# Performance work log

Hardware: AMD Instinct MI355X
Metric: run time of the kernel (lower is better)

## Reference

```python
import jax, jax.numpy as jnp
import numpy as np

N = 20000      # nodes
E = 400000     # edges
D = 256        # input_dim == hidden_dim
L = 4          # num_layers
EIN = 32       # edgenet_input_dim // 2
EH = 128       # edge parser hidden
NC = 2         # num_classes
JK = L * D     # 1024
BN_EPS = 1e-5


def setup_inputs() -> dict:
    key = jax.random.key(0)
    ks = jax.random.split(key, 16)
    s = 0.05
    inp = {
        "features": jax.random.normal(ks[0], (N, D), jnp.float32),
        "edge_index": jax.random.randint(ks[1], (2, E), 0, N, dtype=jnp.int64),
        "edgenet_input": jax.random.normal(ks[2], (E, 2 * EIN), jnp.float32),
        # ChebConv weights: [layer, k, in, out] (all layers 256->256, K=3, no bias)
        "cheb_w": jax.random.normal(ks[3], (L, 3, D, D), jnp.float32) * s,
        # EdgeEncoder (PAE-style) parser: Linear(32,128)+ReLU+BN+Linear(128,128)
        "en_w1": jax.random.normal(ks[4], (EIN, EH), jnp.float32) * s,
        "en_b1": jnp.zeros((EH,), jnp.float32),
        "en_g1": jnp.ones((EH,), jnp.float32),
        "en_be1": jnp.zeros((EH,), jnp.float32),
        "en_w2": jax.random.normal(ks[5], (EH, EH), jnp.float32) * s,
        "en_b2": jnp.zeros((EH,), jnp.float32),
        # cls head: Linear(1024,256)+ReLU+BN(256)+Linear(256,2)
        "cls_w1": jax.random.normal(ks[6], (JK, 256), jnp.float32) * s,
        "cls_b1": jnp.zeros((256,), jnp.float32),
        "cls_g": jnp.ones((256,), jnp.float32),
        "cls_b": jnp.zeros((256,), jnp.float32),
        "cls_w2": jax.random.normal(ks[7], (256, NC), jnp.float32) * s,
        "cls_b2": jnp.zeros((NC,), jnp.float32),
    }
    return inp


def _bn_eval(x, g, b):
    # eval-mode BatchNorm1d with fresh running stats (mean=0, var=1)
    return x * (g / jnp.sqrt(1.0 + BN_EPS)) + b


def reference(features, edge_index, edgenet_input, cheb_w,
              en_w1, en_b1, en_g1, en_be1, en_w2, en_b2,
              cls_w1, cls_b1, cls_g, cls_b, cls_w2, cls_b2):
    row, col = edge_index[0], edge_index[1]

    # ---- EdgeEncoder (PAE): shared parser on both halves + cosine sim ----
    def parser(x):
        h = jnp.maximum(x @ en_w1 + en_b1, 0.0)
        h = _bn_eval(h, en_g1, en_be1)
        return h @ en_w2 + en_b2

    half = edgenet_input.shape[1] // 2
    h1 = parser(edgenet_input[:, :half])
    h2 = parser(edgenet_input[:, half:])
    n1 = jnp.maximum(jnp.linalg.norm(h1, axis=1), 1e-8)
    n2 = jnp.maximum(jnp.linalg.norm(h2, axis=1), 1e-8)
    cos = jnp.sum(h1 * h2, axis=1) / (n1 * n2)
    edge_weight = (cos + 1.0) * 0.5  # [E]

    # ---- ChebConv sym normalization (lambda_max=2): L_hat = -D^-1/2 A D^-1/2 ----
    deg = jax.ops.segment_sum(edge_weight, row, num_segments=N)
    dis = jnp.where(deg > 0, jax.lax.rsqrt(jnp.maximum(deg, 1e-30)), 0.0)
    norm = -dis[row] * edge_weight * dis[col]  # [E]

    def prop(x):  # out[col] += norm * x[row]
        return jax.ops.segment_sum(x[row] * norm[:, None], col, num_segments=N)

    # ---- stacked ChebConv (K=3, no bias) + ReLU + JK concat ----
    x = features
    jk = None
    for i in range(L):
        W = cheb_w[i]
        Tx0 = x
        Tx1 = prop(Tx0)
        Tx2 = 2.0 * prop(Tx1) - Tx0
        h = jnp.maximum(Tx0 @ W[0] + Tx1 @ W[1] + Tx2 @ W[2], 0.0)
        jk = h if i == 0 else jnp.concatenate([jk, h], axis=1)
        x = h

    # ---- cls head ----
    z = jnp.maximum(jk @ cls_w1 + cls_b1, 0.0)
    z = _bn_eval(z, cls_g, cls_b)
    logit = z @ cls_w2 + cls_b2
    return (logit, edge_weight)
```

## Files before the change

### kernel.cpp

```cpp
#include <hip/hip_runtime.h>
#include <hip/hip_bf16.h>

#define NN 20000
#define EE 400000
#define RSBN 0.9999950000374997f

typedef __attribute__((ext_vector_type(8))) short short8;
typedef __attribute__((ext_vector_type(8))) unsigned short ushort8;
typedef __attribute__((ext_vector_type(4))) short bf4;
typedef __attribute__((ext_vector_type(4))) float floatx4;

__device__ __forceinline__ short f2bf(float f) {
  union { float f; unsigned u; } v; v.f = f;
  unsigned r = v.u + 0x7fffu + ((v.u >> 16) & 1u);
  return (short)(r >> 16);
}
__device__ __forceinline__ unsigned f2bf2(float x, float y) {
  union { __hip_bfloat162 h; unsigned u; } v;
  v.h = __float22bfloat162_rn(make_float2(x, y));
  return v.u;
}
__device__ __forceinline__ float bf2f(unsigned short u) {
  union { unsigned u; float f; } v; v.u = ((unsigned)u) << 16;
  return v.f;
}
__device__ __forceinline__ void gl_lds16(const void* g, void* l) {
  __builtin_amdgcn_global_load_lds(
      (const __attribute__((address_space(1))) unsigned*)g,
      (__attribute__((address_space(3))) unsigned*)l, 16, 0, 0);
}

__device__ __forceinline__ floatx4 mfma16(bf4 a, bf4 b, floatx4 c) {
#if __has_builtin(__builtin_amdgcn_mfma_f32_16x16x16bf16_1k)
  return __builtin_amdgcn_mfma_f32_16x16x16bf16_1k(a, b, c, 0, 0, 0);
#else
  floatx4 d;
  asm volatile("v_mfma_f32_16x16x16_bf16 %0, %1, %2, %3"
               : "=&v"(d) : "v"(a), "v"(b), "v"(c));
  return d;
#endif
}

__global__ __launch_bounds__(256) void ewconv_kernel(
    const float* __restrict__ w1, const float* __restrict__ w2,
    const float* __restrict__ g1, const float* __restrict__ be1,
    const float* __restrict__ b1, const float* __restrict__ b2,
    unsigned short* __restrict__ ewf)
{
  int tid = threadIdx.x;
#pragma unroll
  for (int i = 0; i < 16; i++) {
    int idx = i * 256 + tid;
    int k = idx >> 7, n = idx & 127;
    int pos = ((n >> 4) * 64 + (k >> 3) * 16 + (n & 15)) * 8 + (k & 7);
    ewf[pos] = f2bf(w1[idx]);
  }
#pragma unroll
  for (int i = 0; i < 64; i++) {
    int idx = i * 256 + tid;
    int k = idx >> 7, n = idx & 127;
    int u = k >> 4, q = (k >> 2) & 3, j = k & 3;
    int t = n >> 4, l = n & 15;
    int pos = (((u * 8 + t) * 4 + q) * 16 + l) * 4 + j;
    ewf[4096 + pos] = f2bf(w2[idx] * g1[k] * RSBN);
  }
  float* fb = (float*)(ewf + 20480);
  if (tid < 128) {
    fb[tid] = b1[tid];
    float acc = b2[tid];
    for (int k = 0; k < 128; k++) acc += be1[k] * w2[k * 128 + tid] * g1[k] * RSBN;
    fb[128 + tid] = acc;
  }
}

__global__ __launch_bounds__(512, 6) void edge_kernel(
    const float* __restrict__ xin, const int* __restrict__ eidx,
    const unsigned short* __restrict__ ewf,
    float* __restrict__ ew_out,
    float* __restrict__ deg, int* __restrict__ cnt)
{
  __shared__ short wbuf[20992];

  int tid = threadIdx.x;
  int lane = tid & 63;
  int wv = tid >> 6;
  int l15 = lane & 15;
  int quad = lane >> 4;

#pragma unroll
  for (int i = 0; i < 5; i++)
    gl_lds16(ewf + (i * 512 + tid) * 8, &wbuf[(i * 512 + tid) * 8]);
  if (tid < 64)
    gl_lds16(ewf + (2560 + tid) * 8, &wbuf[(2560 + tid) * 8]);

  const short* w1f = wbuf;
  const short* w2f = wbuf + 4096;

  int rowbase = blockIdx.x * 128 + wv * 16;

  short8 af;
  {
    const float* xp = xin + (size_t)(rowbase + l15) * 32 + quad * 8;
    float4 v0 = *(const float4*)xp;
    float4 v1 = *(const float4*)(xp + 4);
    union { short8 s; unsigned u[4]; } a;
    a.u[0] = f2bf2(v0.x, v0.y); a.u[1] = f2bf2(v0.z, v0.w);
    a.u[2] = f2bf2(v1.x, v1.y); a.u[3] = f2bf2(v1.z, v1.w);
    af = a.s;
  }

  __syncthreads();

  const float* fb = (const float*)(wbuf + 20480);

  floatx4 acc1[8];
#pragma unroll
  for (int t = 0; t < 8; t++) {
    floatx4 z = *(const floatx4*)&fb[t * 16 + quad * 4];
    acc1[t] = __builtin_amdgcn_mfma_f32_16x16x32_bf16(
        *(const short8*)&w1f[(t * 64 + lane) * 8], af, z, 0, 0, 0);
  }

  bf4 pb[8];
#pragma unroll
  for (int u = 0; u < 8; u++) {
    union { bf4 s; unsigned w[2]; } o;
    o.w[0] = f2bf2(fmaxf(acc1[u][0], 0.f), fmaxf(acc1[u][1], 0.f));
    o.w[1] = f2bf2(fmaxf(acc1[u][2], 0.f), fmaxf(acc1[u][3], 0.f));
    pb[u] = o.s;
  }

  floatx4 acc2[8];
#pragma unroll
  for (int t = 0; t < 8; t++)
    acc2[t] = *(const floatx4*)&fb[128 + t * 16 + quad * 4];
#pragma unroll
  for (int u = 0; u < 8; u++)
#pragma unroll
    for (int t = 0; t < 8; t++) {
      bf4 a4 = *(const bf4*)&w2f[((u * 8 + t) * 64 + lane) * 4];
      acc2[t] = mfma16(a4, pb[u], acc2[t]);
    }

  float qq = 0.f, pp = 0.f;
#pragma unroll
  for (int t = 0; t < 8; t++)
#pragma unroll
    for (int r = 0; r < 4; r++) {
      float h = acc2[t][r];
      float hp = __shfl_xor(h, 1, 64);
      qq += h * h;
      pp += h * hp;
    }
  qq += __shfl_xor(qq, 16, 64);
  pp += __shfl_xor(pp, 16, 64);
  qq += __shfl_xor(qq, 32, 64);
  pp += __shfl_xor(pp, 32, 64);
  float rr = __shfl_xor(qq, 1, 64);

  if (quad == 0 && !(l15 & 1)) {
    int e = (rowbase + l15) >> 1;
    float n1 = fmaxf(sqrtf(qq), 1e-8f);
    float n2 = fmaxf(sqrtf(rr), 1e-8f);
    float w = (pp / (n1 * n2) + 1.f) * 0.5f;
    ew_out[e] = w;
    atomicAdd(deg + eidx[e], w);
    atomicAdd(cnt + eidx[EE + e], 1);
  }
}

__global__ __launch_bounds__(256) void fconv_kernel(const float* __restrict__ src,
                                                    unsigned short* __restrict__ dst) {
  size_t i = ((size_t)blockIdx.x * 256 + threadIdx.x) * 8;
  float4 a = *(const float4*)(src + i);
  float4 b = *(const float4*)(src + i + 4);
  union { ushort8 s; unsigned u[4]; } o;
  o.u[0] = f2bf2(a.x, a.y); o.u[1] = f2bf2(a.z, a.w);
  o.u[2] = f2bf2(b.x, b.y); o.u[3] = f2bf2(b.z, b.w);
  *(ushort8*)(dst + i) = o.s;
}

__global__ __launch_bounds__(256) void wconv_kernel(
    const float* __restrict__ cheb_w, const float* __restrict__ cls_w1,
    unsigned short* __restrict__ wtc, unsigned short* __restrict__ clsT)
{
  __shared__ unsigned short tile[64][80];
  int z = blockIdx.z;
  const float* src; unsigned short* dst; int ldk;
  if (z < 12) {
    int l = z / 3, c = z % 3;
    src = cheb_w + (size_t)z * 65536;
    dst = wtc + (size_t)l * 196608 + c * 256;
    ldk = 768;
  } else {
    int c = z - 12;
    src = cls_w1 + (size_t)c * 65536;
    dst = clsT + c * 256;
    ldk = 1024;
  }
  int t = threadIdx.x;
  int k0 = blockIdx.x * 64, n0 = blockIdx.y * 64;
#pragma unroll
  for (int pass = 0; pass < 4; pass++) {
    int kk = pass * 16 + (t >> 4);
    int nl = (t & 15) * 4;
    float4 v = *(const float4*)(src + (size_t)(k0 + kk) * 256 + n0 + nl);
    tile[nl + 0][kk] = f2bf(v.x);
    tile[nl + 1][kk] = f2bf(v.y);
    tile[nl + 2][kk] = f2bf(v.z);
    tile[nl + 3][kk] = f2bf(v.w);
  }
  __syncthreads();
  int nl = t >> 2, kc = (t & 3) * 16;
  ushort8 v0 = *(const ushort8*)&tile[nl][kc];
  ushort8 v1 = *(const ushort8*)&tile[nl][kc + 8];
  unsigned short* dp = dst + (size_t)(n0 + nl) * ldk + k0 + kc;
  *(ushort8*)dp = v0;
  *(ushort8*)(dp + 8) = v1;
}

__global__ __launch_bounds__(1024) void scan_kernel(const int* __restrict__ cnt, int* __restrict__ ptr) {
  __shared__ int sums[1024];
  int tid = threadIdx.x;
  const int n = NN;
  const int chunk = (n + 1023) / 1024;
  int base = tid * chunk;
  int s = 0;
  for (int i = 0; i < chunk; i++) {
    int idx = base + i;
    if (idx < n) s += (cnt[idx] + 3) & ~3;
  }
  sums[tid] = s;
  __syncthreads();
  for (int off = 1; off < 1024; off <<= 1) {
    int v = (tid >= off) ? sums[tid - off] : 0;
    __syncthreads();
    sums[tid] += v;
    __syncthreads();
  }
  int run = (tid == 0) ? 0 : sums[tid - 1];
  for (int i = 0; i < chunk; i++) {
    int idx = base + i;
    if (idx < n) { ptr[idx] = run; run += (cnt[idx] + 3) & ~3; }
  }
  if (tid == 1023) ptr[n] = run;
}

__global__ void fill_kernel(const int* __restrict__ eidx, const float* __restrict__ ew,
                            const float* __restrict__ deg, const int* __restrict__ ptr,
                            int* __restrict__ fill, int* __restrict__ cidx, float* __restrict__ cval) {
  int e = blockIdx.x * 256 + threadIdx.x;
  if (e < EE) {
    int r = eidx[e], c = eidx[EE + e];
    float dr = deg[r], dc = deg[c];
    float ir = dr > 0.f ? 1.f / sqrtf(fmaxf(dr, 1e-30f)) : 0.f;
    float ic = dc > 0.f ? 1.f / sqrtf(fmaxf(dc, 1e-30f)) : 0.f;
    float nv = -ir * ew[e] * ic;
    int pos = ptr[c] + atomicAdd(&fill[c], 1);
    cidx[pos] = r;
    cval[pos] = nv;
  }
}

__global__ __launch_bounds__(256) void prop_kernel(
    const unsigned short* __restrict__ x, int ldx,
    const int* __restrict__ cidx, const float* __restrict__ cval,
    const int* __restrict__ ptr,
    unsigned short* __restrict__ y, int ldy,
    float alpha, const unsigned short* __restrict__ sub, int ldsub)
{
  int sliceid = blockIdx.x & 7;
  int colslice = sliceid >> 1;
  int chunk = (blockIdx.x >> 3) * 2 + (sliceid & 1);
  int c = chunk * 32 + (threadIdx.x >> 3);
  if (c >= NN) return;
  int d = colslice * 64 + (threadIdx.x & 7) * 8;
  int p0 = ptr[c], p1 = ptr[c + 1];
  float a[8] = {0.f, 0.f, 0.f, 0.f, 0.f, 0.f, 0.f, 0.f};
  if (p0 < p1) {
    int4 r4 = *(const int4*)(cidx + p0);
    float4 w4 = *(const float4*)(cval + p0);
    ushort8 v0 = *(const ushort8*)(x + (size_t)r4.x * ldx + d);
    ushort8 v1 = *(const ushort8*)(x + (size_t)r4.y * ldx + d);
    ushort8 v2 = *(const ushort8*)(x + (size_t)r4.z * ldx + d);
    ushort8 v3 = *(const ushort8*)(x + (size_t)r4.w * ldx + d);
    for (int p = p0 + 4; p < p1; p += 4) {
      int4 r4n = *(const int4*)(cidx + p);
      float4 w4n = *(const float4*)(cval + p);
      ushort8 n0 = *(const ushort8*)(x + (size_t)r4n.x * ldx + d);
      ushort8 n1 = *(const ushort8*)(x + (size_t)r4n.y * ldx + d);
      ushort8 n2 = *(const ushort8*)(x + (size_t)r4n.z * ldx + d);
      ushort8 n3 = *(const ushort8*)(x + (size_t)r4n.w * ldx + d);
#pragma unroll
      for (int j = 0; j < 8; j++)
        a[j] += w4.x * bf2f(v0[j]) + w4.y * bf2f(v1[j]) + w4.z * bf2f(v2[j]) + w4.w * bf2f(v3[j]);
      w4 = w4n; v0 = n0; v1 = n1; v2 = n2; v3 = n3;
    }
#pragma unroll
    for (int j = 0; j < 8; j++)
      a[j] += w4.x * bf2f(v0[j]) + w4.y * bf2f(v1[j]) + w4.z * bf2f(v2[j]) + w4.w * bf2f(v3[j]);
  }
  union { ushort8 s; unsigned u[4]; } o;
  if (sub) {
    ushort8 sv = *(const ushort8*)(sub + (size_t)c * ldsub + d);
#pragma unroll
    for (int j = 0; j < 8; j += 2)
      o.u[j >> 1] = f2bf2(alpha * a[j] - bf2f(sv[j]), alpha * a[j + 1] - bf2f(sv[j + 1]));
  } else {
#pragma unroll
    for (int j = 0; j < 8; j += 2)
      o.u[j >> 1] = f2bf2(a[j], a[j + 1]);
  }
  *(ushort8*)(y + (size_t)c * ldy + d) = o.s;
}

__global__ __launch_bounds__(256, 4) void mgemm_kernel(
    const unsigned short* A0, const unsigned short* A1,
    const unsigned short* A2, const unsigned short* A3,
    int l0, int l1, int l2, int l3, int nchunks,
    const unsigned short* __restrict__ BT, int ldbt,
    unsigned short* __restrict__ Cb, float* __restrict__ Cf, int ldc, int M,
    const float* __restrict__ bias, const float* __restrict__ bng,
    const float* __restrict__ bnb)
{
  __shared__ short As[4 * 64 * 8];
  __shared__ short Bs[4 * 128 * 8];
  int tid = threadIdx.x;
  int lane = tid & 63;
  int wv = tid >> 6;
  int l15 = lane & 15, quad = lane >> 4;
  int wr = wv >> 1, wc = wv & 1;
  int m0 = blockIdx.x * 64, n0 = blockIdx.y * 128;

  const unsigned short* Ap[4] = {A0, A1, A2, A3};
  int Al[4] = {l0, l1, l2, l3};

  int arow = tid & 63, ac = tid >> 6;
  int brow = tid & 127, bc = tid >> 7;

  floatx4 acc[2][4];
#pragma unroll
  for (int mi = 0; mi < 2; mi++)
#pragma unroll
    for (int nj = 0; nj < 4; nj++) acc[mi][nj] = (floatx4){0.f, 0.f, 0.f, 0.f};

  for (int c = 0; c < nchunks; c++) {
    const unsigned short* Abase = Ap[c] + (size_t)(m0 + arow) * Al[c] + ac * 8;
    const unsigned short* Bbase = BT + (size_t)(n0 + brow) * ldbt + c * 256 + bc * 8;
#pragma unroll 1
    for (int kb = 0; kb < 256; kb += 32) {
      __syncthreads();
      gl_lds16(Abase + kb, &As[tid * 8]);
      gl_lds16(Bbase + kb, &Bs[tid * 8]);
      gl_lds16(Bbase + 16 + kb, &Bs[(tid + 256) * 8]);
      __syncthreads();
      short8 af[2], bfv[4];
#pragma unroll
      for (int mi = 0; mi < 2; mi++)
        af[mi] = *(const short8*)&As[(quad * 64 + wr * 32 + mi * 16 + l15) * 8];
#pragma unroll
      for (int nj = 0; nj < 4; nj++)
        bfv[nj] = *(const short8*)&Bs[(quad * 128 + wc * 64 + nj * 16 + l15) * 8];
#pragma unroll
      for (int nj = 0; nj < 4; nj++)
#pragma unroll
        for (int mi = 0; mi < 2; mi++)
          acc[mi][nj] = __builtin_amdgcn_mfma_f32_16x16x32_bf16(af[mi], bfv[nj], acc[mi][nj], 0, 0, 0);
    }
  }

  if (Cb) {
#pragma unroll
    for (int mi = 0; mi < 2; mi++)
#pragma unroll
      for (int r = 0; r < 4; r++) {
        int row = m0 + wr * 32 + mi * 16 + quad * 4 + r;
        if (row < M) {
#pragma unroll
          for (int nj = 0; nj < 4; nj++) {
            int col = n0 + wc * 64 + nj * 16 + l15;
            Cb[(size_t)row * ldc + col] = (unsigned short)f2bf(fmaxf(acc[mi][nj][r], 0.f));
          }
        }
      }
  } else {
    float bs[4], g[4], bb[4];
#pragma unroll
    for (int nj = 0; nj < 4; nj++) {
      int col = n0 + wc * 64 + nj * 16 + l15;
      bs[nj] = bias[col]; g[nj] = bng[col] * RSBN; bb[nj] = bnb[col];
    }
#pragma unroll
    for (int mi = 0; mi < 2; mi++)
#pragma unroll
      for (int r = 0; r < 4; r++) {
        int row = m0 + wr * 32 + mi * 16 + quad * 4 + r;
        if (row < M) {
#pragma unroll
          for (int nj = 0; nj < 4; nj++) {
            int col = n0 + wc * 64 + nj * 16 + l15;
            float v = fmaxf(acc[mi][nj][r] + bs[nj], 0.f) * g[nj] + bb[nj];
            Cf[(size_t)row * ldc + col] = v;
          }
        }
      }
  }
}

__global__ __launch_bounds__(256) void logit_kernel(
    const float* __restrict__ z, const float* __restrict__ w2,
    const float* __restrict__ b2, float* __restrict__ out)
{
  int node = blockIdx.x * 4 + (threadIdx.x >> 6);
  if (node >= NN) return;
  int lane = threadIdx.x & 63;
  int k = lane * 4;
  float4 zv = *(const float4*)(z + (size_t)node * 256 + k);
  float4 wa = *(const float4*)(w2 + k * 2);
  float4 wb = *(const float4*)(w2 + k * 2 + 4);
  float a0 = zv.x * wa.x + zv.y * wa.z + zv.z * wb.x + zv.w * wb.z;
  float a1 = zv.x * wa.y + zv.y * wa.w + zv.z * wb.y + zv.w * wb.w;
#pragma unroll
  for (int m = 32; m >= 1; m >>= 1) {
    a0 += __shfl_xor(a0, m, 64);
    a1 += __shfl_xor(a1, m, 64);
  }
  if (lane == 0) {
    out[(size_t)node * 2]     = a0 + b2[0];
    out[(size_t)node * 2 + 1] = a1 + b2[1];
  }
}

extern "C" void kernel_launch(void* const* d_in, const int* in_sizes, int n_in,
                              void* d_out, int out_size, void* d_ws, size_t ws_size,
                              hipStream_t stream) {
  const float* features = (const float*)d_in[0];
  const int*   eidx     = (const int*)d_in[1];
  const float* xin      = (const float*)d_in[2];
  const float* cheb_w   = (const float*)d_in[3];
  const float* en_w1    = (const float*)d_in[4];
  const float* en_b1    = (const float*)d_in[5];
  const float* en_g1    = (const float*)d_in[6];
  const float* en_be1   = (const float*)d_in[7];
  const float* en_w2    = (const float*)d_in[8];
  const float* en_b2    = (const float*)d_in[9];
  const float* cls_w1   = (const float*)d_in[10];
  const float* cls_b1   = (const float*)d_in[11];
  const float* cls_g    = (const float*)d_in[12];
  const float* cls_b    = (const float*)d_in[13];
  const float* cls_w2   = (const float*)d_in[14];
  const float* cls_b2   = (const float*)d_in[15];
  float* out = (float*)d_out;

  char* ws = (char*)d_ws;
  size_t off = 0;
  auto alloc = [&](size_t bytes) -> void* {
    void* p = ws + off;
    off += (bytes + 255) & ~(size_t)255;
    return p;
  };
  const int CSRN = EE + 4 * NN;
  float* deg  = (float*)alloc((size_t)NN * 4);
  int*   cnt  = (int*)  alloc((size_t)NN * 4);
  int*   fil  = (int*)  alloc((size_t)NN * 4);
  float* cval = (float*)alloc((size_t)CSRN * 4);
  int*   cidx = (int*)  alloc((size_t)CSRN * 4);
  size_t zero_len = off;
  int*   ptr  = (int*)  alloc((size_t)(NN + 1) * 4);
  unsigned short* featb = (unsigned short*)alloc((size_t)NN * 256 * 2);
  unsigned short* Tx1   = (unsigned short*)alloc((size_t)NN * 256 * 2);
  unsigned short* Tx2   = (unsigned short*)alloc((size_t)NN * 256 * 2);
  unsigned short* jk    = (unsigned short*)alloc((size_t)NN * 1024 * 2);
  float* zbuf = (float*)alloc((size_t)NN * 256 * 4);
  unsigned short* wtc   = (unsigned short*)alloc((size_t)4 * 196608 * 2);
  unsigned short* clsT  = (unsigned short*)alloc((size_t)256 * 1024 * 2);
  unsigned short* ewf   = (unsigned short*)alloc((size_t)20992 * 2);
  alloc(262144);

  float* ew = out + (size_t)NN * 2;

  hipMemsetAsync(deg, 0, zero_len, stream);

  ewconv_kernel<<<1, 256, 0, stream>>>(en_w1, en_w2, en_g1, en_be1, en_b1, en_b2, ewf);
  edge_kernel<<<6250, 512, 0, stream>>>(xin, eidx, ewf, ew, deg, cnt);
  fconv_kernel<<<2500, 256, 0, stream>>>(features, featb);
  wconv_kernel<<<dim3(4, 4, 16), 256, 0, stream>>>(cheb_w, cls_w1, wtc, clsT);
  scan_kernel<<<1, 1024, 0, stream>>>(cnt, ptr);
  fill_kernel<<<(EE + 255) / 256, 256, 0, stream>>>(eidx, ew, deg, ptr, fil, cidx, cval);

  dim3 ggrid(313, 2);
  for (int i = 0; i < 4; i++) {
    const unsigned short* x = (i == 0) ? featb : (jk + (size_t)(i - 1) * 256);
    int ldx = (i == 0) ? 256 : 1024;
    prop_kernel<<<2504, 256, 0, stream>>>(x, ldx, cidx, cval, ptr, Tx1, 256, 1.f, nullptr, 0);
    prop_kernel<<<2504, 256, 0, stream>>>(Tx1, 256, cidx, cval, ptr, Tx2, 256, 2.f, x, ldx);
    mgemm_kernel<<<ggrid, 256, 0, stream>>>(x, Tx1, Tx2, nullptr, ldx, 256, 256, 0, 3,
                                            wtc + (size_t)i * 196608, 768,
                                            jk + (size_t)i * 256, nullptr, 1024, NN,
                                            nullptr, nullptr, nullptr);
  }

  mgemm_kernel<<<ggrid, 256, 0, stream>>>(jk, jk + 256, jk + 512, jk + 768,
                                          1024, 1024, 1024, 1024, 4, clsT, 1024,
                                          nullptr, zbuf, 256, NN,
                                          cls_b1, cls_g, cls_b);
  logit_kernel<<<NN / 4, 256, 0, stream>>>(zbuf, cls_w2, cls_b2, out);
}
```

Baseline: 646.1 us.

## Persistent edge-encoder blocks with prefetch and deeper K tile in mgemm

The edge encoder kernel now has each block process five 128-row tiles in a loop, with 1250 blocks instead of 6250. This spreads the cost of loading the weight tile into LDS over more rows and prefetches the next tile's inputs while the current one computes. The mgemm kernel doubles the K step per LDS stage from 32 to 64, which halves the barrier count and the number of load iterations. The price is double the shared memory per GEMM block, which may reduce occupancy, and fewer edge blocks, which may leave some compute units underused.

```diff
diff --git a/kernel.cpp b/kernel.cpp
--- a/kernel.cpp
+++ b/kernel.cpp
@@ -96,76 +96,95 @@
   const short* w1f = wbuf;
   const short* w2f = wbuf + 4096;
 
-  int rowbase = blockIdx.x * 128 + wv * 16;
-
-  short8 af;
+  int rowbase0 = blockIdx.x * 640 + wv * 16;
+
+  float4 c0, c1;
   {
-    const float* xp = xin + (size_t)(rowbase + l15) * 32 + quad * 8;
-    float4 v0 = *(const float4*)xp;
-    float4 v1 = *(const float4*)(xp + 4);
-    union { short8 s; unsigned u[4]; } a;
-    a.u[0] = f2bf2(v0.x, v0.y); a.u[1] = f2bf2(v0.z, v0.w);
-    a.u[2] = f2bf2(v1.x, v1.y); a.u[3] = f2bf2(v1.z, v1.w);
-    af = a.s;
+    const float* xp = xin + (size_t)(rowbase0 + l15) * 32 + quad * 8;
+    c0 = *(const float4*)xp;
+    c1 = *(const float4*)(xp + 4);
   }
 
   __syncthreads();
 
   const float* fb = (const float*)(wbuf + 20480);
 
-  floatx4 acc1[8];
-#pragma unroll
-  for (int t = 0; t < 8; t++) {
-    floatx4 z = *(const floatx4*)&fb[t * 16 + quad * 4];
-    acc1[t] = __builtin_amdgcn_mfma_f32_16x16x32_bf16(
-        *(const short8*)&w1f[(t * 64 + lane) * 8], af, z, 0, 0, 0);
-  }
-
-  bf4 pb[8];
-#pragma unroll
-  for (int u = 0; u < 8; u++) {
-    union { bf4 s; unsigned w[2]; } o;
-    o.w[0] = f2bf2(fmaxf(acc1[u][0], 0.f), fmaxf(acc1[u][1], 0.f));
-    o.w[1] = f2bf2(fmaxf(acc1[u][2], 0.f), fmaxf(acc1[u][3], 0.f));
-    pb[u] = o.s;
-  }
-
-  floatx4 acc2[8];
-#pragma unroll
-  for (int t = 0; t < 8; t++)
-    acc2[t] = *(const floatx4*)&fb[128 + t * 16 + quad * 4];
-#pragma unroll
-  for (int u = 0; u < 8; u++)
-#pragma unroll
-    for (int t = 0; t < 8; t++) {
-      bf4 a4 = *(const bf4*)&w2f[((u * 8 + t) * 64 + lane) * 4];
-      acc2[t] = mfma16(a4, pb[u], acc2[t]);
-    }
-
-  float qq = 0.f, pp = 0.f;
-#pragma unroll
-  for (int t = 0; t < 8; t++)
-#pragma unroll
-    for (int r = 0; r < 4; r++) {
-      float h = acc2[t][r];
-      float hp = __shfl_xor(h, 1, 64);
-      qq += h * h;
-      pp += h * hp;
-    }
-  qq += __shfl_xor(qq, 16, 64);
-  pp += __shfl_xor(pp, 16, 64);
-  qq += __shfl_xor(qq, 32, 64);
-  pp += __shfl_xor(pp, 32, 64);
-  float rr = __shfl_xor(qq, 1, 64);
-
-  if (quad == 0 && !(l15 & 1)) {
+#pragma unroll 1
+  for (int t = 0; t < 5; t++) {
+    int rowbase = rowbase0 + t * 128;
+
+    float4 n0, n1;
+    if (t < 4) {
+      const float* np = xin + (size_t)(rowbase + 128 + l15) * 32 + quad * 8;
+      n0 = *(const float4*)np;
+      n1 = *(const float4*)(np + 4);
+    }
     int e = (rowbase + l15) >> 1;
-    float n1 = fmaxf(sqrtf(qq), 1e-8f);
-    float n2 = fmaxf(sqrtf(rr), 1e-8f);
-    float w = (pp / (n1 * n2) + 1.f) * 0.5f;
-    ew_out[e] = w;
-    atomicAdd(deg + eidx[e], w);
-    atomicAdd(cnt + eidx[EE + e], 1);
+    int er = eidx[e], ec = eidx[EE + e];
+
+    short8 af;
+    {
+      union { short8 s; unsigned u[4]; } a;
+      a.u[0] = f2bf2(c0.x, c0.y); a.u[1] = f2bf2(c0.z, c0.w);
+      a.u[2] = f2bf2(c1.x, c1.y); a.u[3] = f2bf2(c1.z, c1.w);
+      af = a.s;
+    }
+
+    floatx4 acc1[8];
+#pragma unroll
+    for (int u = 0; u < 8; u++) {
+      floatx4 z = *(const floatx4*)&fb[u * 16 + quad * 4];
+      acc1[u] = __builtin_amdgcn_mfma_f32_16x16x32_bf16(
+          *(const short8*)&w1f[(u * 64 + lane) * 8], af, z, 0, 0, 0);
+    }
+
+    bf4 pb[8];
+#pragma unroll
+    for (int u = 0; u < 8; u++) {
+      union { bf4 s; unsigned w[2]; } o;
+      o.w[0] = f2bf2(fmaxf(acc1[u][0], 0.f), fmaxf(acc1[u][1], 0.f));
+      o.w[1] = f2bf2(fmaxf(acc1[u][2], 0.f), fmaxf(acc1[u][3], 0.f));
+      pb[u] = o.s;
+    }
+
+    floatx4 acc2[8];
+#pragma unroll
+    for (int u = 0; u < 8; u++)
+      acc2[u] = *(const floatx4*)&fb[128 + u * 16 + quad * 4];
+#pragma unroll
+    for (int u = 0; u < 8; u++)
+#pragma unroll
+      for (int v = 0; v < 8; v++) {
+        bf4 a4 = *(const bf4*)&w2f[((u * 8 + v) * 64 + lane) * 4];
+        acc2[v] = mfma16(a4, pb[u], acc2[v]);
+      }
+
+    float qq = 0.f, pp = 0.f;
+#pragma unroll
+    for (int v = 0; v < 8; v++)
+#pragma unroll
+      for (int r = 0; r < 4; r++) {
+        float h = acc2[v][r];
+        float hp = __shfl_xor(h, 1, 64);
+        qq += h * h;
+        pp += h * hp;
+      }
+    qq += __shfl_xor(qq, 16, 64);
+    pp += __shfl_xor(pp, 16, 64);
+    qq += __shfl_xor(qq, 32, 64);
+    pp += __shfl_xor(pp, 32, 64);
+    float rr = __shfl_xor(qq, 1, 64);
+
+    if (quad == 0 && !(l15 & 1)) {
+      float n1v = fmaxf(sqrtf(qq), 1e-8f);
+      float n2v = fmaxf(sqrtf(rr), 1e-8f);
+      float w = (pp / (n1v * n2v) + 1.f) * 0.5f;
+      ew_out[e] = w;
+      atomicAdd(deg + er, w);
+      atomicAdd(cnt + ec, 1);
+    }
+
+    if (t < 4) { c0 = n0; c1 = n1; }
   }
 }
 
@@ -323,8 +342,8 @@
     const float* __restrict__ bias, const float* __restrict__ bng,
     const float* __restrict__ bnb)
 {
-  __shared__ short As[4 * 64 * 8];
-  __shared__ short Bs[4 * 128 * 8];
+  __shared__ short As[8 * 64 * 8];
+  __shared__ short Bs[8 * 128 * 8];
   int tid = threadIdx.x;
   int lane = tid & 63;
   int wv = tid >> 6;
@@ -346,26 +365,34 @@
 
   for (int c = 0; c < nchunks; c++) {
     const unsigned short* Abase = Ap[c] + (size_t)(m0 + arow) * Al[c] + ac * 8;
-    const unsigned short* Bbase = BT + (size_t)(n0 + brow) * ldbt + c * 256 + bc * 8;
+    const unsigned short* Bbase = BT + (size_t)(n0 + brow) * ldbt + c * 256;
 #pragma unroll 1
-    for (int kb = 0; kb < 256; kb += 32) {
+    for (int kb = 0; kb < 256; kb += 64) {
       __syncthreads();
-      gl_lds16(Abase + kb, &As[tid * 8]);
-      gl_lds16(Bbase + kb, &Bs[tid * 8]);
-      gl_lds16(Bbase + 16 + kb, &Bs[(tid + 256) * 8]);
+      gl_lds16(Abase + kb,      &As[(ac * 64 + arow) * 8]);
+      gl_lds16(Abase + kb + 32, &As[((ac + 4) * 64 + arow) * 8]);
+#pragma unroll
+      for (int h = 0; h < 4; h++) {
+        int kc = bc + 2 * h;
+        int ko = (kc & 3) * 8 + (kc >> 2) * 32;
+        gl_lds16(Bbase + kb + ko, &Bs[(kc * 128 + brow) * 8]);
+      }
       __syncthreads();
-      short8 af[2], bfv[4];
-#pragma unroll
-      for (int mi = 0; mi < 2; mi++)
-        af[mi] = *(const short8*)&As[(quad * 64 + wr * 32 + mi * 16 + l15) * 8];
-#pragma unroll
-      for (int nj = 0; nj < 4; nj++)
-        bfv[nj] = *(const short8*)&Bs[(quad * 128 + wc * 64 + nj * 16 + l15) * 8];
-#pragma unroll
-      for (int nj = 0; nj < 4; nj++)
+#pragma unroll
+      for (int s = 0; s < 2; s++) {
+        short8 af[2], bfv[4];
 #pragma unroll
         for (int mi = 0; mi < 2; mi++)
-          acc[mi][nj] = __builtin_amdgcn_mfma_f32_16x16x32_bf16(af[mi], bfv[nj], acc[mi][nj], 0, 0, 0);
+          af[mi] = *(const short8*)&As[((s * 4 + quad) * 64 + wr * 32 + mi * 16 + l15) * 8];
+#pragma unroll
+        for (int nj = 0; nj < 4; nj++)
+          bfv[nj] = *(const short8*)&Bs[((s * 4 + quad) * 128 + wc * 64 + nj * 16 + l15) * 8];
+#pragma unroll
+        for (int nj = 0; nj < 4; nj++)
+#pragma unroll
+          for (int mi = 0; mi < 2; mi++)
+            acc[mi][nj] = __builtin_amdgcn_mfma_f32_16x16x32_bf16(af[mi], bfv[nj], acc[mi][nj], 0, 0, 0);
+      }
     }
   }
 
@@ -482,7 +509,7 @@
   hipMemsetAsync(deg, 0, zero_len, stream);
 
   ewconv_kernel<<<1, 256, 0, stream>>>(en_w1, en_w2, en_g1, en_be1, en_b1, en_b2, ewf);
-  edge_kernel<<<6250, 512, 0, stream>>>(xin, eidx, ewf, ew, deg, cnt);
+  edge_kernel<<<1250, 512, 0, stream>>>(xin, eidx, ewf, ew, deg, cnt);
   fconv_kernel<<<2500, 256, 0, stream>>>(features, featb);
   wconv_kernel<<<dim3(4, 4, 16), 256, 0, stream>>>(cheb_w, cls_w1, wtc, clsT);
   scan_kernel<<<1, 1024, 0, stream>>>(cnt, ptr);
```

Measured after the change: 1.248 ms. +93.2%, slower.
